# Kernel optimization log

Hardware: AMD Instinct MI355X
Metric: run time of the kernel (lower is better)

Reference implementation:

```python
import jax, jax.numpy as jnp
import numpy as np

FEAT_DIM = 128  # used for the 1/sqrt(2*feat_dim) attention scale, per the source
_DN = ('NCHW', 'OIHW', 'NCHW')


def _conv_block(x, w1, b1, w2, b2):
    # Conv2d(k=3, stride=1, pad=0) -> ReLU -> Conv2d(k=3) -> ReLU
    h = jax.lax.conv_general_dilated(x, w1, (1, 1), 'VALID', dimension_numbers=_DN)
    h = jax.nn.relu(h + b1[None, :, None, None])
    h = jax.lax.conv_general_dilated(h, w2, (1, 1), 'VALID', dimension_numbers=_DN)
    return jax.nn.relu(h + b2[None, :, None, None])


def setup_inputs() -> dict:
    key = jax.random.key(0)
    ks = jax.random.split(key, 16)
    E, C, H, W = 2048, 16, 16, 16
    G, N = 16, 128  # 16 graphs x 128 edges
    fd = FEAT_DIM
    edge_feat = jax.random.normal(ks[0], (E, C, H, W), dtype=jnp.float32)
    edge_graph_id = (jnp.arange(E) // N).astype(jnp.int64)  # sorted, equal-size groups

    def conv_w(k, out_c, in_c):
        std = 1.0 / np.sqrt(in_c * 9)
        return jax.random.normal(k, (out_c, in_c, 3, 3), dtype=jnp.float32) * std

    inp = {'edge_feat': edge_feat, 'edge_graph_id': edge_graph_id}
    i = 1
    for name in ('q', 'k', 'v'):
        inp[f'{name}_w1'] = conv_w(ks[i], fd, C)
        inp[f'{name}_b1'] = jnp.zeros((fd,), dtype=jnp.float32)
        inp[f'{name}_w2'] = conv_w(ks[i + 1], fd, fd)
        inp[f'{name}_b2'] = jnp.zeros((fd,), dtype=jnp.float32)
        i += 2
    return inp


def reference(edge_feat, edge_graph_id,
              q_w1, q_b1, q_w2, q_b2,
              k_w1, k_b1, k_w2, k_b2,
              v_w1, v_b1, v_w2, v_b2):
    q = _conv_block(edge_feat, q_w1, q_b1, q_w2, q_b2)  # [E, 128, 12, 12]
    k = _conv_block(edge_feat, k_w1, k_b1, k_w2, k_b2)
    v = _conv_block(edge_feat, v_w1, v_b1, v_w2, v_b2)
    E = q.shape[0]
    feat_shape = q.shape[-3:]
    G = int(edge_graph_id[-1]) + 1  # sorted contiguous equal-size groups
    D = feat_shape[0] * feat_shape[1] * feat_shape[2]
    qf = q.reshape(G, E // G, D)
    kf = k.reshape(G, E // G, D)
    vf = v.reshape(G, E // G, D)
    scale = 1.0 / np.sqrt(2 * FEAT_DIM).astype(np.float32)
    attn = jax.nn.softmax(jnp.einsum('gnd,gmd->gnm', qf, kf) * scale, axis=-1)
    out = jnp.einsum('gnm,gmd->gnd', attn, vf)
    return out.reshape(E, *feat_shape)
```

## Files before the change

### kernel.cpp

```cpp
#include <hip/hip_runtime.h>
#include <hip/hip_bf16.h>

typedef unsigned short u16;
typedef unsigned int   u32;

typedef __bf16 bf16x8 __attribute__((ext_vector_type(8)));
typedef float  f32x4  __attribute__((ext_vector_type(4)));

struct alignas(16) US8  { u16 s[8]; };
struct alignas(8)  US4  { u16 s[4]; };
struct alignas(16) UI4  { u32 d[4]; };
struct alignas(8)  U32x2{ u32 x, y; };

__device__ __forceinline__ u16 f2bf(float f) {
  u32 x = __builtin_bit_cast(u32, f);
  return (u16)((x + 0x7fffu + ((x >> 16) & 1u)) >> 16);
}
__device__ __forceinline__ u32 cvtpk(float a, float b) {
  u32 r;
  asm("v_cvt_pk_bf16_f32 %0, %1, %2" : "=v"(r) : "v"(a), "v"(b));
  return r;
}
__device__ __forceinline__ bf16x8 ld8(const u16* p) {
  return __builtin_bit_cast(bf16x8, *(const US8*)p);
}
__device__ __forceinline__ f32x4 mfma16(bf16x8 a, bf16x8 b, f32x4 c) {
  return __builtin_amdgcn_mfma_f32_16x16x32_bf16(a, b, c, 0, 0, 0);
}
__device__ __forceinline__ f32x4 zero4() { f32x4 z; z[0]=0.f; z[1]=0.f; z[2]=0.f; z[3]=0.f; return z; }

#define NE     2048
#define DFULL  18432
#define XROWB 800

__global__ void prep_weights(const float* __restrict__ w1q, const float* __restrict__ w1k, const float* __restrict__ w1v,
                             const float* __restrict__ w2q, const float* __restrict__ w2k, const float* __restrict__ w2v,
                             u16* __restrict__ w1p, u16* __restrict__ w2p)
{
  int idx = blockIdx.x * blockDim.x + threadIdx.x;
  int stride = gridDim.x * blockDim.x;
  for (int i = idx; i < 3*128*160; i += stride) {
    int b = i / (128*160); int r = i % (128*160);
    int oc = r / 160, k = r % 160;
    u16 v = 0;
    if (k < 144) {
      int kk = k >> 4, ic = k & 15;
      const float* w = (b == 0) ? w1q : (b == 1) ? w1k : w1v;
      v = f2bf(w[oc*144 + ic*9 + kk]);
    }
    w1p[i] = v;
  }
  for (int i = idx; i < 3*128*1152; i += stride) {
    int b = i / (128*1152); int r = i % (128*1152);
    int oc = r / 1152, k = r % 1152;
    int kk = k >> 7, ic = k & 127;
    const float* w = (b == 0) ? w2q : (b == 1) ? w2k : w2v;
    w2p[i] = f2bf(w[oc*1152 + ic*9 + kk]);
  }
}

__global__ __launch_bounds__(256, 2)
void conv_fused(const float* __restrict__ edge_feat,
                const u16* __restrict__ w1p, const u16* __restrict__ w2p,
                const float* __restrict__ b1q, const float* __restrict__ b1k, const float* __restrict__ b1v,
                const float* __restrict__ b2q, const float* __restrict__ b2k, const float* __restrict__ b2v,
                u16* __restrict__ outq, u16* __restrict__ outk, u16* __restrict__ outv)
{
  const int bb = blockIdx.x / NE;
  const int e  = blockIdx.x % NE;
  const int t = threadIdx.x;
  const int w = t >> 6, l = t & 63;
  const int l15 = l & 15, lq = l >> 4;

  __shared__ __align__(16) u16 x_hwc[6416];
  __shared__ __align__(16) u16 h1t[196 * 128];
  __shared__ float b1f[128], b2f[128];

  {
    const float* xin = edge_feat + (size_t)e * 4096 + t;
    float v[16];
    #pragma unroll
    for (int c = 0; c < 16; ++c) v[c] = xin[c*256];
    UI4 lo_, hi_;
    #pragma unroll
    for (int i = 0; i < 4; ++i) lo_.d[i] = cvtpk(v[2*i],   v[2*i+1]);
    #pragma unroll
    for (int i = 0; i < 4; ++i) hi_.d[i] = cvtpk(v[8+2*i], v[8+2*i+1]);
    int base = (t >> 4)*400 + (t & 15)*24;
    *(UI4*)(x_hwc + base)     = lo_;
    *(UI4*)(x_hwc + base + 8) = hi_;
  }
  {
    const float* b1p = bb == 0 ? b1q : bb == 1 ? b1k : b1v;
    const float* b2p = bb == 0 ? b2q : bb == 1 ? b2k : b2v;
    if (t < 128) { b1f[t] = b1p[t]; b2f[t] = b2p[t]; }
    if (t < 8) x_hwc[6400 + t] = 0;
  }
  __syncthreads();

  const u16* W1b = w1p + bb * (128*160);
  f32x4 acc1[2][13];
  #pragma unroll
  for (int mi = 0; mi < 2; ++mi)
    #pragma unroll
    for (int nt = 0; nt < 13; ++nt) acc1[mi][nt] = zero4();

  int offb[13];
  #pragma unroll
  for (int nt = 0; nt < 13; ++nt) {
    int p = nt*16 + l15; if (p > 195) p = 195;
    int y = p / 14, x = p % 14;
    offb[nt] = y*XROWB + x*48;
  }

  #pragma unroll
  for (int ks = 0; ks < 5; ++ks) {
    int k = ks*32 + lq*8;
    bf16x8 a0 = ld8(W1b + ((w*2 + 0)*16 + l15)*160 + k);
    bf16x8 a1 = ld8(W1b + ((w*2 + 1)*16 + l15)*160 + k);
    int kk = k >> 4;
    int ky = kk / 3, kx = kk - ky*3;
    int koffB = ky*XROWB + kx*48 + (k & 15)*2;
    bool kvalid = (k < 144);
    #pragma unroll
    for (int nt = 0; nt < 13; ++nt) {
      int byte = kvalid ? (offb[nt] + koffB) : 12800;
      bf16x8 bf = ld8((const u16*)((const char*)x_hwc + byte));
      acc1[0][nt] = mfma16(a0, bf, acc1[0][nt]);
      acc1[1][nt] = mfma16(a1, bf, acc1[1][nt]);
    }
  }

  {
    int oc0 = lq*4;
    #pragma unroll
    for (int mi = 0; mi < 2; ++mi) {
      int ocb = (w*2 + mi)*16 + oc0;
      #pragma unroll
      for (int nt = 0; nt < 13; ++nt) {
        int p = nt*16 + l15;
        if (p < 196) {
          float r0 = acc1[mi][nt][0] + b1f[ocb+0]; r0 = r0 > 0.f ? r0 : 0.f;
          float r1 = acc1[mi][nt][1] + b1f[ocb+1]; r1 = r1 > 0.f ? r1 : 0.f;
          float r2 = acc1[mi][nt][2] + b1f[ocb+2]; r2 = r2 > 0.f ? r2 : 0.f;
          float r3 = acc1[mi][nt][3] + b1f[ocb+3]; r3 = r3 > 0.f ? r3 : 0.f;
          U32x2 val{ cvtpk(r0, r1), cvtpk(r2, r3) };
          int byte = p*256 + ((ocb*2) ^ ((p & 7) << 4));
          *(U32x2*)((char*)h1t + byte) = val;
        }
      }
    }
  }
  __syncthreads();

  int ppb[9], p2o[9];
  #pragma unroll
  for (int nt = 0; nt < 9; ++nt) {
    int y2, x2;
    if (nt < 6) { y2 = nt + 6*(l15 >> 3); x2 = l15 & 7; }
    else        { y2 = (nt-6)*4 + (l15 & 3); x2 = 8 + (l15 >> 2); }
    ppb[nt] = y2*14 + x2;
    p2o[nt] = y2*12 + x2;
  }

  const u16* W2b = w2p + bb * (128*1152);
  f32x4 acc2[2][9];
  #pragma unroll
  for (int mi = 0; mi < 2; ++mi)
    #pragma unroll
    for (int nt = 0; nt < 9; ++nt) acc2[mi][nt] = zero4();

  const u16* A0p = W2b + ((w*2 + 0)*16 + l15)*1152;
  const u16* A1p = W2b + ((w*2 + 1)*16 + l15)*1152;
  bf16x8 a0 = ld8(A0p + lq*8);
  bf16x8 a1 = ld8(A1p + lq*8);
  const int lq16 = lq*16;

  #pragma unroll
  for (int kk = 0; kk < 9; ++kk) {
    int ky = kk / 3, kx = kk - ky*3;
    int pkp = ky*14 + kx;
    int ax[9];
    #pragma unroll
    for (int nt = 0; nt < 9; ++nt) {
      int pp = ppb[nt] + pkp;
      ax[nt] = pp*256 + (lq16 ^ ((pp & 7) << 4));
    }
    #pragma unroll
    for (int s = 0; s < 4; ++s) {
      int ks = kk*4 + s;
      int k = ks*32 + lq*8;
      int kn = (ks < 35) ? (k + 32) : (lq*8);
      bf16x8 na0 = ld8(A0p + kn);
      bf16x8 na1 = ld8(A1p + kn);
      int kx6 = s << 6;
      #pragma unroll
      for (int nt = 0; nt < 9; ++nt) {
        bf16x8 bfr = ld8((const u16*)((const char*)h1t + (ax[nt] ^ kx6)));
        acc2[0][nt] = mfma16(a0, bfr, acc2[0][nt]);
        acc2[1][nt] = mfma16(a1, bfr, acc2[1][nt]);
      }
      a0 = na0; a1 = na1;
    }
  }

  u16* outp = bb == 0 ? outq : bb == 1 ? outk : outv;
  u16* oe = outp + (size_t)e * DFULL;
  #pragma unroll
  for (int mi = 0; mi < 2; ++mi) {
    int ocb = (w*2 + mi)*16 + lq*4;
    #pragma unroll
    for (int nt = 0; nt < 9; ++nt) {
      #pragma unroll
      for (int r = 0; r < 4; ++r) {
        float v = acc2[mi][nt][r] + b2f[ocb + r];
        v = v > 0.f ? v : 0.f;
        oe[(ocb + r)*144 + p2o[nt]] = f2bf(v);
      }
    }
  }
}

__global__ __launch_bounds__(256, 2)
void qk_partial(const u16* __restrict__ Q, const u16* __restrict__ K, float* __restrict__ Sp, int nc)
{
  const int g = blockIdx.x / nc, kc = blockIdx.x % nc;
  const int t = threadIdx.x, w = t >> 6, l = t & 63;
  const int l15 = l & 15, lq = l >> 4;
  const int CH = DFULL / nc;
  const u16* Qb = Q + (size_t)g*128*DFULL + kc*CH;
  const u16* Kb = K + (size_t)g*128*DFULL + kc*CH;

  f32x4 acc[2][8];
  #pragma unroll
  for (int mi = 0; mi < 2; ++mi)
    #pragma unroll
    for (int nt = 0; nt < 8; ++nt) acc[mi][nt] = zero4();

  for (int ks = 0; ks < CH/32; ++ks) {
    int k = ks*32 + lq*8;
    bf16x8 a0 = ld8(Qb + (size_t)((w*2 + 0)*16 + l15)*DFULL + k);
    bf16x8 a1 = ld8(Qb + (size_t)((w*2 + 1)*16 + l15)*DFULL + k);
    #pragma unroll
    for (int nt = 0; nt < 8; ++nt) {
      bf16x8 b = ld8(Kb + (size_t)(nt*16 + l15)*DFULL + k);
      acc[0][nt] = mfma16(a0, b, acc[0][nt]);
      acc[1][nt] = mfma16(a1, b, acc[1][nt]);
    }
  }

  float* So = Sp + (size_t)(g*nc + kc)*16384;
  #pragma unroll
  for (int mi = 0; mi < 2; ++mi)
    #pragma unroll
    for (int nt = 0; nt < 8; ++nt) {
      int col = nt*16 + l15;
      #pragma unroll
      for (int r = 0; r < 4; ++r) {
        int row = (w*2 + mi)*16 + lq*4 + r;
        So[row*128 + col] = acc[mi][nt][r];
      }
    }
}

__global__ void softmax_p(const float* __restrict__ Sp, u16* __restrict__ P, int nc)
{
  const int rr = blockIdx.x;
  const int g = rr >> 7, n = rr & 127;
  const int l = threadIdx.x;
  const float* base = Sp + (size_t)g*nc*16384 + n*128;
  float v0 = 0.f, v1 = 0.f;
  for (int kc = 0; kc < nc; ++kc) {
    v0 += base[(size_t)kc*16384 + l];
    v1 += base[(size_t)kc*16384 + 64 + l];
  }
  v0 *= 0.0625f; v1 *= 0.0625f;
  float m = fmaxf(v0, v1);
  #pragma unroll
  for (int s = 32; s; s >>= 1) m = fmaxf(m, __shfl_xor(m, s));
  float e0 = __expf(v0 - m), e1 = __expf(v1 - m);
  float sum = e0 + e1;
  #pragma unroll
  for (int s = 32; s; s >>= 1) sum += __shfl_xor(sum, s);
  float inv = 1.f / sum;
  u16* Pr = P + (size_t)g*16384 + n*128;
  Pr[l]      = f2bf(e0 * inv);
  Pr[64 + l] = f2bf(e1 * inv);
}

__global__ __launch_bounds__(256, 2)
void pv_kernel(const u16* __restrict__ P, const u16* __restrict__ V, float* __restrict__ O)
{
  const int g  = blockIdx.x / 96;
  const int dc = blockIdx.x % 96;
  const int d0 = dc * 192;
  const int t = threadIdx.x, w = t >> 6, l = t & 63;
  const int l15 = l & 15, lq = l >> 4;

  __shared__ __align__(16) u16 Vl[128 * 196];

  const u16* Vg = V + (size_t)g*128*DFULL + d0;
  for (int i = t; i < 6144; i += 256) {
    int m = i / 48, c4 = (i % 48) * 4;
    *(US4*)(Vl + m*196 + c4) = *(const US4*)(Vg + (size_t)m*DFULL + c4);
  }
  __syncthreads();

  const u16* Pg = P + (size_t)g*16384;
  f32x4 acc[2][12];
  #pragma unroll
  for (int mi = 0; mi < 2; ++mi)
    #pragma unroll
    for (int nt = 0; nt < 12; ++nt) acc[mi][nt] = zero4();

  #pragma unroll
  for (int ks = 0; ks < 4; ++ks) {
    int k = ks*32 + lq*8;
    bf16x8 a0 = ld8(Pg + ((w*2 + 0)*16 + l15)*128 + k);
    bf16x8 a1 = ld8(Pg + ((w*2 + 1)*16 + l15)*128 + k);
    #pragma unroll
    for (int nt = 0; nt < 12; ++nt) {
      int d = nt*16 + l15;
      US8 tmp;
      #pragma unroll
      for (int j = 0; j < 8; ++j) tmp.s[j] = Vl[(k + j)*196 + d];
      bf16x8 b = __builtin_bit_cast(bf16x8, tmp);
      acc[0][nt] = mfma16(a0, b, acc[0][nt]);
      acc[1][nt] = mfma16(a1, b, acc[1][nt]);
    }
  }

  float* Og = O + (size_t)g*128*DFULL + d0;
  #pragma unroll
  for (int mi = 0; mi < 2; ++mi)
    #pragma unroll
    for (int nt = 0; nt < 12; ++nt) {
      int d = nt*16 + l15;
      #pragma unroll
      for (int r = 0; r < 4; ++r) {
        int n = (w*2 + mi)*16 + lq*4 + r;
        Og[(size_t)n*DFULL + d] = acc[mi][nt][r];
      }
    }
}

extern "C" void kernel_launch(void* const* d_in, const int* in_sizes, int n_in,
                              void* d_out, int out_size, void* d_ws, size_t ws_size,
                              hipStream_t stream)
{
  const float* edge_feat = (const float*)d_in[0];
  const float* qw1 = (const float*)d_in[2];
  const float* qb1 = (const float*)d_in[3];
  const float* qw2 = (const float*)d_in[4];
  const float* qb2 = (const float*)d_in[5];
  const float* kw1 = (const float*)d_in[6];
  const float* kb1 = (const float*)d_in[7];
  const float* kw2 = (const float*)d_in[8];
  const float* kb2 = (const float*)d_in[9];
  const float* vw1 = (const float*)d_in[10];
  const float* vb1 = (const float*)d_in[11];
  const float* vw2 = (const float*)d_in[12];
  const float* vb2 = (const float*)d_in[13];

  u16* Qd = (u16*)d_out;
  u16* Kd = (u16*)d_out + (size_t)NE*DFULL;

  char* ws = (char*)d_ws;
  u16*   W1p = (u16*)  (ws + 0);
  u16*   W2p = (u16*)  (ws + 122880);
  u16*   Vb  = (u16*)  (ws + 1007616);
  float* Sp  = (float*)(ws + 76505088);
  int nc = 16;
  size_t need16 = 76505088ull + (size_t)16*16*16384*4 + 524288;
  if (ws_size < need16) nc = 8;
  u16* P = (u16*)(ws + 76505088 + (size_t)16*nc*16384*4);

  prep_weights<<<240, 256, 0, stream>>>(qw1, kw1, vw1, qw2, kw2, vw2, W1p, W2p);
  conv_fused<<<3*NE, 256, 0, stream>>>(edge_feat, W1p, W2p,
                                       qb1, kb1, vb1, qb2, kb2, vb2,
                                       Qd, Kd, Vb);
  qk_partial<<<16*nc, 256, 0, stream>>>(Qd, Kd, Sp, nc);
  softmax_p<<<2048, 64, 0, stream>>>(Sp, P, nc);
  pv_kernel<<<16*96, 256, 0, stream>>>(P, Vb, (float*)d_out);
}
```

Measured before the change: 431.5 us.

## Split conv intermediate into two channel passes to halve LDS and raise occupancy

The fused conv kernel now computes the first conv's 128 output channels in two passes of 64. Each pass writes a half-width h1 tile to shared memory and accumulates the second conv over that K-slice before the next pass. This halves the h1 LDS buffer and shrinks first-conv accumulators (7 tiles at a time instead of 2x13), allowing launch bounds of 3 blocks per CU. In exchange it adds an extra barrier pair per pass, reloads the x tile for each pass, and widens the zero pad region for per-lane pad addressing.

```diff
diff --git a/kernel.cpp b/kernel.cpp
--- a/kernel.cpp
+++ b/kernel.cpp
@@ -59,7 +59,7 @@
   }
 }
 
-__global__ __launch_bounds__(256, 2)
+__global__ __launch_bounds__(256, 3)
 void conv_fused(const float* __restrict__ edge_feat,
                 const u16* __restrict__ w1p, const u16* __restrict__ w2p,
                 const float* __restrict__ b1q, const float* __restrict__ b1k, const float* __restrict__ b1v,
@@ -72,8 +72,8 @@
   const int w = t >> 6, l = t & 63;
   const int l15 = l & 15, lq = l >> 4;
 
-  __shared__ __align__(16) u16 x_hwc[6416];
-  __shared__ __align__(16) u16 h1t[196 * 128];
+  __shared__ __align__(16) u16 x_hwc[6528];
+  __shared__ __align__(16) u16 h1t[196 * 64];
   __shared__ float b1f[128], b2f[128];
 
   {
@@ -94,16 +94,12 @@
     const float* b1p = bb == 0 ? b1q : bb == 1 ? b1k : b1v;
     const float* b2p = bb == 0 ? b2q : bb == 1 ? b2k : b2v;
     if (t < 128) { b1f[t] = b1p[t]; b2f[t] = b2p[t]; }
-    if (t < 8) x_hwc[6400 + t] = 0;
+    if (t < 128) x_hwc[6400 + t] = 0;
   }
   __syncthreads();
 
   const u16* W1b = w1p + bb * (128*160);
-  f32x4 acc1[2][13];
-  #pragma unroll
-  for (int mi = 0; mi < 2; ++mi)
-    #pragma unroll
-    for (int nt = 0; nt < 13; ++nt) acc1[mi][nt] = zero4();
+  const u16* W2b = w2p + bb * (128*1152);
 
   int offb[13];
   #pragma unroll
@@ -112,96 +108,103 @@
     int y = p / 14, x = p % 14;
     offb[nt] = y*XROWB + x*48;
   }
-
-  #pragma unroll
-  for (int ks = 0; ks < 5; ++ks) {
-    int k = ks*32 + lq*8;
-    bf16x8 a0 = ld8(W1b + ((w*2 + 0)*16 + l15)*160 + k);
-    bf16x8 a1 = ld8(W1b + ((w*2 + 1)*16 + l15)*160 + k);
-    int kk = k >> 4;
-    int ky = kk / 3, kx = kk - ky*3;
-    int koffB = ky*XROWB + kx*48 + (k & 15)*2;
-    bool kvalid = (k < 144);
-    #pragma unroll
-    for (int nt = 0; nt < 13; ++nt) {
-      int byte = kvalid ? (offb[nt] + koffB) : 12800;
-      bf16x8 bf = ld8((const u16*)((const char*)x_hwc + byte));
-      acc1[0][nt] = mfma16(a0, bf, acc1[0][nt]);
-      acc1[1][nt] = mfma16(a1, bf, acc1[1][nt]);
-    }
-  }
-
-  {
-    int oc0 = lq*4;
-    #pragma unroll
-    for (int mi = 0; mi < 2; ++mi) {
-      int ocb = (w*2 + mi)*16 + oc0;
-      #pragma unroll
-      for (int nt = 0; nt < 13; ++nt) {
-        int p = nt*16 + l15;
-        if (p < 196) {
-          float r0 = acc1[mi][nt][0] + b1f[ocb+0]; r0 = r0 > 0.f ? r0 : 0.f;
-          float r1 = acc1[mi][nt][1] + b1f[ocb+1]; r1 = r1 > 0.f ? r1 : 0.f;
-          float r2 = acc1[mi][nt][2] + b1f[ocb+2]; r2 = r2 > 0.f ? r2 : 0.f;
-          float r3 = acc1[mi][nt][3] + b1f[ocb+3]; r3 = r3 > 0.f ? r3 : 0.f;
-          U32x2 val{ cvtpk(r0, r1), cvtpk(r2, r3) };
-          int byte = p*256 + ((ocb*2) ^ ((p & 7) << 4));
-          *(U32x2*)((char*)h1t + byte) = val;
-        }
-      }
-    }
-  }
-  __syncthreads();
-
-  int ppb[9], p2o[9];
+  const int padB = 12800 + l15*16;
+
+  int ppb[9];
   #pragma unroll
   for (int nt = 0; nt < 9; ++nt) {
     int y2, x2;
     if (nt < 6) { y2 = nt + 6*(l15 >> 3); x2 = l15 & 7; }
     else        { y2 = (nt-6)*4 + (l15 & 3); x2 = 8 + (l15 >> 2); }
     ppb[nt] = y2*14 + x2;
-    p2o[nt] = y2*12 + x2;
-  }
-
-  const u16* W2b = w2p + bb * (128*1152);
+  }
+  const int lq16 = lq*16;
+
   f32x4 acc2[2][9];
   #pragma unroll
   for (int mi = 0; mi < 2; ++mi)
     #pragma unroll
     for (int nt = 0; nt < 9; ++nt) acc2[mi][nt] = zero4();
 
-  const u16* A0p = W2b + ((w*2 + 0)*16 + l15)*1152;
-  const u16* A1p = W2b + ((w*2 + 1)*16 + l15)*1152;
-  bf16x8 a0 = ld8(A0p + lq*8);
-  bf16x8 a1 = ld8(A1p + lq*8);
-  const int lq16 = lq*16;
-
-  #pragma unroll
-  for (int kk = 0; kk < 9; ++kk) {
-    int ky = kk / 3, kx = kk - ky*3;
-    int pkp = ky*14 + kx;
-    int ax[9];
-    #pragma unroll
-    for (int nt = 0; nt < 9; ++nt) {
-      int pp = ppb[nt] + pkp;
-      ax[nt] = pp*256 + (lq16 ^ ((pp & 7) << 4));
-    }
-    #pragma unroll
-    for (int s = 0; s < 4; ++s) {
-      int ks = kk*4 + s;
-      int k = ks*32 + lq*8;
-      int kn = (ks < 35) ? (k + 32) : (lq*8);
-      bf16x8 na0 = ld8(A0p + kn);
-      bf16x8 na1 = ld8(A1p + kn);
-      int kx6 = s << 6;
+  #pragma unroll
+  for (int pass = 0; pass < 2; ++pass) {
+    const u16* A1 = W1b + (pass*64 + w*16 + l15)*160;
+    const int oclb = w*16 + lq*4;
+    #pragma unroll
+    for (int half = 0; half < 2; ++half) {
+      const int n0 = half ? 7 : 0;
+      const int nn = half ? 6 : 7;
+      f32x4 acc1[7];
+      #pragma unroll
+      for (int i = 0; i < 7; ++i) acc1[i] = zero4();
+      #pragma unroll
+      for (int ks = 0; ks < 5; ++ks) {
+        int k = ks*32 + lq*8;
+        bf16x8 a = ld8(A1 + k);
+        int kk = k >> 4;
+        int ky = kk / 3, kx = kk - ky*3;
+        int koffB = ky*XROWB + kx*48 + (k & 15)*2;
+        bool kvalid = (k < 144);
+        #pragma unroll
+        for (int i = 0; i < 7; ++i) {
+          if (i < nn) {
+            int byte = kvalid ? (offb[n0 + i] + koffB) : padB;
+            bf16x8 bf = ld8((const u16*)((const char*)x_hwc + byte));
+            acc1[i] = mfma16(a, bf, acc1[i]);
+          }
+        }
+      }
+      #pragma unroll
+      for (int i = 0; i < 7; ++i) {
+        if (i < nn) {
+          int p = (n0 + i)*16 + l15;
+          if (p < 196) {
+            int ocg = pass*64 + oclb;
+            float r0 = acc1[i][0] + b1f[ocg+0]; r0 = r0 > 0.f ? r0 : 0.f;
+            float r1 = acc1[i][1] + b1f[ocg+1]; r1 = r1 > 0.f ? r1 : 0.f;
+            float r2 = acc1[i][2] + b1f[ocg+2]; r2 = r2 > 0.f ? r2 : 0.f;
+            float r3 = acc1[i][3] + b1f[ocg+3]; r3 = r3 > 0.f ? r3 : 0.f;
+            U32x2 val{ cvtpk(r0, r1), cvtpk(r2, r3) };
+            int byte = p*128 + ((oclb*2) ^ ((p & 7) << 4));
+            *(U32x2*)((char*)h1t + byte) = val;
+          }
+        }
+      }
+    }
+    __syncthreads();
+
+    const u16* A0p = W2b + ((w*2 + 0)*16 + l15)*1152 + pass*64;
+    const u16* A1p = W2b + ((w*2 + 1)*16 + l15)*1152 + pass*64;
+    bf16x8 a0 = ld8(A0p + lq*8);
+    bf16x8 a1 = ld8(A1p + lq*8);
+    #pragma unroll
+    for (int kk = 0; kk < 9; ++kk) {
+      int ky = kk / 3, kx = kk - ky*3;
+      int pkp = ky*14 + kx;
+      int ax[9];
       #pragma unroll
       for (int nt = 0; nt < 9; ++nt) {
-        bf16x8 bfr = ld8((const u16*)((const char*)h1t + (ax[nt] ^ kx6)));
-        acc2[0][nt] = mfma16(a0, bfr, acc2[0][nt]);
-        acc2[1][nt] = mfma16(a1, bfr, acc2[1][nt]);
-      }
-      a0 = na0; a1 = na1;
-    }
+        int pp = ppb[nt] + pkp;
+        ax[nt] = pp*128 + (lq16 ^ ((pp & 7) << 4));
+      }
+      #pragma unroll
+      for (int s = 0; s < 2; ++s) {
+        int ks = kk*2 + s;
+        int knext = (ks < 17) ? (ks + 1) : 0;
+        int kncol = (knext >> 1)*128 + (knext & 1)*32 + lq*8;
+        bf16x8 na0 = ld8(A0p + kncol);
+        bf16x8 na1 = ld8(A1p + kncol);
+        int sx = s << 6;
+        #pragma unroll
+        for (int nt = 0; nt < 9; ++nt) {
+          bf16x8 bfr = ld8((const u16*)((const char*)h1t + (ax[nt] ^ sx)));
+          acc2[0][nt] = mfma16(a0, bfr, acc2[0][nt]);
+          acc2[1][nt] = mfma16(a1, bfr, acc2[1][nt]);
+        }
+        a0 = na0; a1 = na1;
+      }
+    }
+    __syncthreads();
   }
 
   u16* outp = bb == 0 ? outq : bb == 1 ? outk : outv;
@@ -211,11 +214,13 @@
     int ocb = (w*2 + mi)*16 + lq*4;
     #pragma unroll
     for (int nt = 0; nt < 9; ++nt) {
+      int y2 = ppb[nt] / 14, x2 = ppb[nt] % 14;
+      int p2o = y2*12 + x2;
       #pragma unroll
       for (int r = 0; r < 4; ++r) {
         float v = acc2[mi][nt][r] + b2f[ocb + r];
         v = v > 0.f ? v : 0.f;
-        oe[(ocb + r)*144 + p2o[nt]] = f2bf(v);
+        oe[(ocb + r)*144 + p2o] = f2bf(v);
       }
     }
   }
```

Measured after the change: 1.598 ms. 270% more time.

## Pre-convert input to bf16 HWC in global memory and read conv1 operands from it

Applied to the files above, without the earlier changes.

Adds a prep_x kernel that converts edge features once to bf16 in HWC layout in a workspace buffer, so each of the three q/k/v conv blocks no longer reconverts fp32 input. With the global path enabled, conv_fused reads conv1 B operands directly from global memory (relying on cache) instead of staging them in LDS, and pads the K tail from a zero buffer. This shrinks LDS use and removes the per-block staging sync, which may raise occupancy, but adds an extra kernel launch and uncoalesced global loads inside the MFMA loop. The workspace is re-laid out to alias Xh with the score buffer, and the old LDS path is kept as a fallback when the workspace is small.

```diff
diff --git a/kernel.cpp b/kernel.cpp
--- a/kernel.cpp
+++ b/kernel.cpp
@@ -31,14 +31,15 @@
 
 #define NE     2048
 #define DFULL  18432
-#define XROWB 800
+#define XROWB  800
 
 __global__ void prep_weights(const float* __restrict__ w1q, const float* __restrict__ w1k, const float* __restrict__ w1v,
                              const float* __restrict__ w2q, const float* __restrict__ w2k, const float* __restrict__ w2v,
-                             u16* __restrict__ w1p, u16* __restrict__ w2p)
+                             u16* __restrict__ w1p, u16* __restrict__ w2p, u16* __restrict__ zbuf)
 {
   int idx = blockIdx.x * blockDim.x + threadIdx.x;
   int stride = gridDim.x * blockDim.x;
+  if (idx < 256) zbuf[idx] = 0;
   for (int i = idx; i < 3*128*160; i += stride) {
     int b = i / (128*160); int r = i % (128*160);
     int oc = r / 160, k = r % 160;
@@ -59,8 +60,27 @@
   }
 }
 
+__global__ void prep_x(const float* __restrict__ ef, u16* __restrict__ Xh)
+{
+  const int e = blockIdx.x, t = threadIdx.x;
+  const float* xin = ef + (size_t)e*4096 + t;
+  float v[16];
+  #pragma unroll
+  for (int c = 0; c < 16; ++c) v[c] = xin[c*256];
+  UI4 lo_, hi_;
+  #pragma unroll
+  for (int i = 0; i < 4; ++i) lo_.d[i] = cvtpk(v[2*i],   v[2*i+1]);
+  #pragma unroll
+  for (int i = 0; i < 4; ++i) hi_.d[i] = cvtpk(v[8+2*i], v[8+2*i+1]);
+  u16* out = Xh + (size_t)e*4096 + t*16;
+  *(UI4*)out       = lo_;
+  *(UI4*)(out + 8) = hi_;
+}
+
+template<int GX>
 __global__ __launch_bounds__(256, 2)
 void conv_fused(const float* __restrict__ edge_feat,
+                const u16* __restrict__ Xh, const u16* __restrict__ zbuf,
                 const u16* __restrict__ w1p, const u16* __restrict__ w2p,
                 const float* __restrict__ b1q, const float* __restrict__ b1k, const float* __restrict__ b1v,
                 const float* __restrict__ b2q, const float* __restrict__ b2k, const float* __restrict__ b2v,
@@ -72,11 +92,11 @@
   const int w = t >> 6, l = t & 63;
   const int l15 = l & 15, lq = l >> 4;
 
-  __shared__ __align__(16) u16 x_hwc[6416];
+  __shared__ __align__(16) u16 x_hwc[GX ? 8 : 6528];
   __shared__ __align__(16) u16 h1t[196 * 128];
   __shared__ float b1f[128], b2f[128];
 
-  {
+  if constexpr (!GX) {
     const float* xin = edge_feat + (size_t)e * 4096 + t;
     float v[16];
     #pragma unroll
@@ -89,12 +109,12 @@
     int base = (t >> 4)*400 + (t & 15)*24;
     *(UI4*)(x_hwc + base)     = lo_;
     *(UI4*)(x_hwc + base + 8) = hi_;
+    if (t < 128) x_hwc[6400 + t] = 0;
   }
   {
     const float* b1p = bb == 0 ? b1q : bb == 1 ? b1k : b1v;
     const float* b2p = bb == 0 ? b2q : bb == 1 ? b2k : b2v;
     if (t < 128) { b1f[t] = b1p[t]; b2f[t] = b2p[t]; }
-    if (t < 8) x_hwc[6400 + t] = 0;
   }
   __syncthreads();
 
@@ -110,24 +130,47 @@
   for (int nt = 0; nt < 13; ++nt) {
     int p = nt*16 + l15; if (p > 195) p = 195;
     int y = p / 14, x = p % 14;
-    offb[nt] = y*XROWB + x*48;
-  }
-
-  #pragma unroll
-  for (int ks = 0; ks < 5; ++ks) {
-    int k = ks*32 + lq*8;
-    bf16x8 a0 = ld8(W1b + ((w*2 + 0)*16 + l15)*160 + k);
-    bf16x8 a1 = ld8(W1b + ((w*2 + 1)*16 + l15)*160 + k);
-    int kk = k >> 4;
-    int ky = kk / 3, kx = kk - ky*3;
-    int koffB = ky*XROWB + kx*48 + (k & 15)*2;
-    bool kvalid = (k < 144);
-    #pragma unroll
-    for (int nt = 0; nt < 13; ++nt) {
-      int byte = kvalid ? (offb[nt] + koffB) : 12800;
-      bf16x8 bf = ld8((const u16*)((const char*)x_hwc + byte));
-      acc1[0][nt] = mfma16(a0, bf, acc1[0][nt]);
-      acc1[1][nt] = mfma16(a1, bf, acc1[1][nt]);
+    offb[nt] = GX ? (y*16 + x)*16
+                  : y*XROWB + x*48;
+  }
+
+  if constexpr (GX) {
+    const u16* XhE = Xh + (size_t)e*4096;
+    const u16* zp  = zbuf + (l & 31)*8;
+    #pragma unroll
+    for (int ks = 0; ks < 5; ++ks) {
+      int k = ks*32 + lq*8;
+      bf16x8 a0 = ld8(W1b + ((w*2 + 0)*16 + l15)*160 + k);
+      bf16x8 a1 = ld8(W1b + ((w*2 + 1)*16 + l15)*160 + k);
+      int kk = k >> 4;
+      int ky = kk / 3, kx = kk - ky*3;
+      int kofft = ky*256 + kx*16 + (k & 15);
+      bool kvalid = (k < 144);
+      #pragma unroll
+      for (int nt = 0; nt < 13; ++nt) {
+        const u16* bp = kvalid ? (XhE + offb[nt] + kofft) : zp;
+        bf16x8 bf = ld8(bp);
+        acc1[0][nt] = mfma16(a0, bf, acc1[0][nt]);
+        acc1[1][nt] = mfma16(a1, bf, acc1[1][nt]);
+      }
+    }
+  } else {
+    #pragma unroll
+    for (int ks = 0; ks < 5; ++ks) {
+      int k = ks*32 + lq*8;
+      bf16x8 a0 = ld8(W1b + ((w*2 + 0)*16 + l15)*160 + k);
+      bf16x8 a1 = ld8(W1b + ((w*2 + 1)*16 + l15)*160 + k);
+      int kk = k >> 4;
+      int ky = kk / 3, kx = kk - ky*3;
+      int koffB = ky*XROWB + kx*48 + (k & 15)*2;
+      bool kvalid = (k < 144);
+      #pragma unroll
+      for (int nt = 0; nt < 13; ++nt) {
+        int byte = kvalid ? (offb[nt] + koffB) : 12800;
+        bf16x8 bf = ld8((const u16*)((const char*)x_hwc + byte));
+        acc1[0][nt] = mfma16(a0, bf, acc1[0][nt]);
+        acc1[1][nt] = mfma16(a1, bf, acc1[1][nt]);
+      }
     }
   }
 
@@ -366,19 +409,30 @@
   u16* Kd = (u16*)d_out + (size_t)NE*DFULL;
 
   char* ws = (char*)d_ws;
-  u16*   W1p = (u16*)  (ws + 0);
-  u16*   W2p = (u16*)  (ws + 122880);
-  u16*   Vb  = (u16*)  (ws + 1007616);
-  float* Sp  = (float*)(ws + 76505088);
-  int nc = 16;
-  size_t need16 = 76505088ull + (size_t)16*16*16384*4 + 524288;
-  if (ws_size < need16) nc = 8;
-  u16* P = (u16*)(ws + 76505088 + (size_t)16*nc*16384*4);
-
-  prep_weights<<<240, 256, 0, stream>>>(qw1, kw1, vw1, qw2, kw2, vw2, W1p, W2p);
-  conv_fused<<<3*NE, 256, 0, stream>>>(edge_feat, W1p, W2p,
-                                       qb1, kb1, vb1, qb2, kb2, vb2,
-                                       Qd, Kd, Vb);
+  u16*   W1p  = (u16*)(ws + 0);
+  u16*   W2p  = (u16*)(ws + 122880);
+  u16*   zbuf = (u16*)(ws + 1007616);
+  u16*   Vb   = (u16*)(ws + 1008640);
+  char*  XhSp = ws + 76506112;
+  u16*   Xh   = (u16*)XhSp;
+  float* Sp   = (float*)XhSp;
+
+  int gx, nc; u16* P;
+  if (ws_size >= 93807616ull)      { gx = 1; nc = 16; P = (u16*)(ws + 93283328); }
+  else if (ws_size >= 93283328ull) { gx = 1; nc = 8;  P = (u16*)(XhSp + 8388608); }
+  else                             { gx = 0; nc = 8;  P = (u16*)(XhSp + 8388608); }
+
+  prep_weights<<<240, 256, 0, stream>>>(qw1, kw1, vw1, qw2, kw2, vw2, W1p, W2p, zbuf);
+  if (gx) {
+    prep_x<<<NE, 256, 0, stream>>>(edge_feat, Xh);
+    conv_fused<1><<<3*NE, 256, 0, stream>>>(edge_feat, Xh, zbuf, W1p, W2p,
+                                            qb1, kb1, vb1, qb2, kb2, vb2,
+                                            Qd, Kd, Vb);
+  } else {
+    conv_fused<0><<<3*NE, 256, 0, stream>>>(edge_feat, Xh, zbuf, W1p, W2p,
+                                            qb1, kb1, vb1, qb2, kb2, vb2,
+                                            Qd, Kd, Vb);
+  }
   qk_partial<<<16*nc, 256, 0, stream>>>(Qd, Kd, Sp, nc);
   softmax_p<<<2048, 64, 0, stream>>>(Sp, P, nc);
   pv_kernel<<<16*96, 256, 0, stream>>>(P, Vb, (float*)d_out);
```

After: 482.4 us. 11.8% more time.
